# Optimization experiments

Hardware: AMD Instinct MI355X
Metric: run time of the kernel (lower is better)

Reference implementation:

```python
import jax, jax.numpy as jnp
import numpy as np

N = 5000
NUM_CLASSES = 81
BBOX_STD = jnp.array([0.1, 0.1, 0.2, 0.2], dtype=jnp.float32)
MIN_CONF = 0.7
MAX_INST = 100
NMS_THR = 0.3


def apply_box_delta(boxes, deltas):
    # boxes: [N,4] (y1,x1,y2,x2); deltas: [N,4] (dy,dx,log(dh),log(dw))
    h = boxes[:, 2] - boxes[:, 0]
    w = boxes[:, 3] - boxes[:, 1]
    cy = boxes[:, 0] + 0.5 * h
    cx = boxes[:, 1] + 0.5 * w
    cy = cy + deltas[:, 0] * h
    cx = cx + deltas[:, 1] * w
    h = h * jnp.exp(deltas[:, 2])
    w = w * jnp.exp(deltas[:, 3])
    y1 = cy - 0.5 * h
    x1 = cx - 0.5 * w
    return jnp.stack([y1, x1, y1 + h, x1 + w], axis=1)


def clip_boxes(boxes, window):
    wy1, wx1, wy2, wx2 = window[0], window[1], window[2], window[3]
    y1 = jnp.clip(boxes[:, 0], wy1, wy2)
    x1 = jnp.clip(boxes[:, 1], wx1, wx2)
    y2 = jnp.clip(boxes[:, 2], wy1, wy2)
    x2 = jnp.clip(boxes[:, 3], wx1, wx2)
    return jnp.stack([y1, x1, y2, x2], axis=1)


def pairwise_iou(boxes):
    # boxes: [N,4] -> iou: [N,N]
    y1, x1, y2, x2 = boxes[:, 0], boxes[:, 1], boxes[:, 2], boxes[:, 3]
    area = jnp.maximum(y2 - y1, 0.0) * jnp.maximum(x2 - x1, 0.0)
    iy1 = jnp.maximum(y1[:, None], y1[None, :])
    ix1 = jnp.maximum(x1[:, None], x1[None, :])
    iy2 = jnp.minimum(y2[:, None], y2[None, :])
    ix2 = jnp.minimum(x2[:, None], x2[None, :])
    inter = jnp.maximum(iy2 - iy1, 0.0) * jnp.maximum(ix2 - ix1, 0.0)
    union = area[:, None] + area[None, :] - inter
    return jnp.where(union > 0.0, inter / jnp.maximum(union, 1e-12), 0.0)


def setup_inputs() -> dict:
    key = jax.random.key(0)
    k1, k2, k3 = jax.random.split(key, 3)
    # valid boxes in normalized coords: (y1,x1) = min corner, (y2,x2) = max corner
    pts = jax.random.uniform(k1, (N, 2, 2), dtype=jnp.float32)
    lo = jnp.min(pts, axis=1)  # [N,2] -> (ymin, xmin)
    hi = jnp.max(pts, axis=1)  # [N,2] -> (ymax, xmax)
    ROIs = jnp.concatenate([lo, hi], axis=1)
    probs = jax.random.uniform(k2, (N, NUM_CLASSES), dtype=jnp.float32)
    deltas = jax.random.normal(k3, (N, NUM_CLASSES, 4), dtype=jnp.float32) * 0.5
    window = jnp.array([0.0, 0.0, 1.0, 1.0], dtype=jnp.float32)
    return {"ROIs": ROIs, "probs": probs, "deltas": deltas, "window": window}


def reference(ROIs, probs, deltas, window):
    n = probs.shape[0]
    rows = jnp.arange(n)
    # compute_delta: top class per ROI, its score and class-specific delta
    class_ids = jnp.argmax(probs, axis=1)
    class_scores = probs[rows, class_ids]
    deltas_specific = deltas[rows, class_ids] * BBOX_STD
    # refine + clip
    refined = clip_boxes(apply_box_delta(ROIs, deltas_specific), window)
    # keep: non-background & above confidence threshold
    valid = (class_ids > 0) & (class_scores >= MIN_CONF)
    # per-class greedy NMS, processed in global descending-score order
    # (identical result to per-unique-class tf.image.non_max_suppression)
    iou = pairwise_iou(refined)  # [N,N]
    neg_inf = jnp.float32(-jnp.inf)
    order = jnp.argsort(-jnp.where(valid, class_scores, neg_inf))

    def step(carry, i):
        kept, counts = carry
        c = class_ids[i]
        suppressed = jnp.any(kept & (class_ids == c) & (iou[i] > NMS_THR))
        ok = valid[i] & (~suppressed) & (counts[c] < MAX_INST)
        kept = kept.at[i].set(ok)
        counts = counts.at[c].add(ok.astype(jnp.int32))
        return (kept, counts), None

    init = (jnp.zeros((n,), dtype=bool), jnp.zeros((NUM_CLASSES,), dtype=jnp.int32))
    (kept, _), _ = jax.lax.scan(step, init, order)
    final = valid & kept
    # top detection_max_instances by score among surviving boxes
    masked_scores = jnp.where(final, class_scores, neg_inf)
    top_scores, top_ids = jax.lax.top_k(masked_scores, MAX_INST)
    ok = top_scores > neg_inf
    det = jnp.concatenate(
        [refined[top_ids],
         class_ids[top_ids].astype(jnp.float32)[:, None],
         class_scores[top_ids][:, None]], axis=1)
    # zero_pad_detections: invalid slots are zero
    return jnp.where(ok[:, None], det, 0.0)  # [MAX_INST, 6]
```

## Files before the change

### kernel.cpp

```cpp
#include <hip/hip_runtime.h>
#include <math.h>

#define NROI 5000
#define NCLS 81
#define MIN_CONF_F 0.7f
#define MAX_INST_I 100
#define NMS_THR_F 0.3f
#define CAP2 128
#define SURV_CAP 8192
#define HBINS 2048
#define CAPF 512
#define BMIN 0x3F333

__global__ __launch_bounds__(256) void det_stage1(
    const float* __restrict__ rois, const float* __restrict__ probs,
    const float* __restrict__ deltas, const float* __restrict__ window,
    float4* __restrict__ g_box, float* __restrict__ g_score,
    int* __restrict__ g_cid, unsigned int* __restrict__ ctrl)
{
  const int gtid = blockIdx.x * blockDim.x + threadIdx.x;
  if (gtid == 0) { ctrl[0] = 0u; ctrl[1] = 0u; }
  const int i = gtid >> 6;
  const int lane = threadIdx.x & 63;
  if (i >= NROI) return;
  const float* p = probs + (size_t)i * NCLS;
  float v0 = p[lane];
  unsigned long long key =
      ((unsigned long long)__float_as_uint(v0) << 32) | (unsigned)(255 - lane);
  if (lane < NCLS - 64) {
    float v1 = p[64 + lane];
    unsigned long long k1 =
        ((unsigned long long)__float_as_uint(v1) << 32) | (unsigned)(255 - (64 + lane));
    if (k1 > key) key = k1;
  }
  #pragma unroll
  for (int off = 32; off > 0; off >>= 1) {
    unsigned long long o = __shfl_xor(key, off, 64);
    if (o > key) key = o;
  }
  if (lane == 0) {
    int bc = 255 - (int)(key & 0xFFull);
    float best = __uint_as_float((unsigned)(key >> 32));
    const float* d = deltas + ((size_t)i * NCLS + bc) * 4;
    float dy = d[0]*0.1f, dx = d[1]*0.1f, dh = d[2]*0.2f, dwv = d[3]*0.2f;
    float y1 = rois[i*4+0], x1 = rois[i*4+1], y2 = rois[i*4+2], x2 = rois[i*4+3];
    float h = y2 - y1, w = x2 - x1;
    float cy = y1 + 0.5f*h, cx = x1 + 0.5f*w;
    cy = cy + dy*h; cx = cx + dx*w;
    h = h*expf(dh); w = w*expf(dwv);
    float ny1 = cy - 0.5f*h, nx1 = cx - 0.5f*w;
    float ny2 = ny1 + h, nx2 = nx1 + w;
    float wy1 = window[0], wx1 = window[1], wy2 = window[2], wx2 = window[3];
    ny1 = fminf(fmaxf(ny1, wy1), wy2);
    nx1 = fminf(fmaxf(nx1, wx1), wx2);
    ny2 = fminf(fmaxf(ny2, wy1), wy2);
    nx2 = fminf(fmaxf(nx2, wx1), wx2);
    g_box[i] = make_float4(ny1, nx1, ny2, nx2);
    g_score[i] = best;
    g_cid[i] = (bc > 0 && best >= MIN_CONF_F) ? bc : -1;
  }
}

__global__ __launch_bounds__(256) void det_nms_topk(
    const float4* __restrict__ g_box, const float* __restrict__ g_score,
    const int* __restrict__ g_cid, unsigned int* __restrict__ ctrl,
    unsigned long long* __restrict__ surv_key, int* __restrict__ surv_cid,
    float* __restrict__ out)
{
  const int c = blockIdx.x + 1;
  const int tid = threadIdx.x;
  __shared__ int scnt;
  __shared__ unsigned long long keys[CAP2], skey[CAP2];
  __shared__ float by1[CAP2], bx1[CAP2], by2[CAP2], bx2[CAP2], barea[CAP2];
  __shared__ unsigned int mask[CAP2][4];
  __shared__ unsigned char skept[CAP2];
  __shared__ int sticket;
  __shared__ int hist[HBINS];
  __shared__ unsigned long long cand[CAPF];
  __shared__ int csrc[CAPF];
  __shared__ float orows[6 * MAX_INST_I];
  __shared__ int wsum[4];
  __shared__ int fcnt, sR;

  if (tid == 0) scnt = 0;
  for (int q = tid; q < CAP2 * 4; q += 256) ((unsigned int*)mask)[q] = 0u;
  if (tid < CAP2) skept[tid] = 0;
  __syncthreads();
  const int4* cid4 = (const int4*)g_cid;
  for (int v = tid; v < NROI / 4; v += 256) {
    int4 cv = cid4[v];
    int base = v * 4;
    #pragma unroll
    for (int q = 0; q < 4; ++q) {
      int cq = (q == 0) ? cv.x : (q == 1) ? cv.y : (q == 2) ? cv.z : cv.w;
      if (cq == c) {
        int i = base + q;
        int pos = atomicAdd(&scnt, 1);
        if (pos < CAP2) {
          unsigned int sb = __float_as_uint(g_score[i]);
          keys[pos] = ((unsigned long long)sb << 32) |
                      (unsigned int)(0xFFFFFFFFu - (unsigned int)i);
        }
      }
    }
  }
  __syncthreads();
  int cnt = scnt < CAP2 ? scnt : CAP2;
  if (cnt > 0) {
    if (tid < cnt) {
      unsigned long long mk = keys[tid];
      int r = 0;
      for (int q = 0; q < cnt; ++q) r += (keys[q] > mk) ? 1 : 0;
      skey[r] = mk;
    }
    __syncthreads();
    if (tid < cnt) {
      int idx = (int)(0xFFFFFFFFu - (unsigned)(skey[tid] & 0xFFFFFFFFull));
      float4 b = g_box[idx];
      by1[tid] = b.x; bx1[tid] = b.y; by2[tid] = b.z; bx2[tid] = b.w;
      barea[tid] = fmaxf(b.z - b.x, 0.0f) * fmaxf(b.w - b.y, 0.0f);
    }
    __syncthreads();
    int m = 1, lg = 0;
    while (m < cnt) { m <<= 1; ++lg; }
    int tot = m * m;
    for (int p = tid; p < tot; p += 256) {
      int j = p >> lg, k = p & (m - 1);
      if (k > j && k < cnt) {
        float iy1 = fmaxf(by1[j], by1[k]);
        float ix1 = fmaxf(bx1[j], bx1[k]);
        float iy2 = fminf(by2[j], by2[k]);
        float ix2 = fminf(bx2[j], bx2[k]);
        float inter = fmaxf(iy2 - iy1, 0.0f) * fmaxf(ix2 - ix1, 0.0f);
        float uni = barea[j] + barea[k] - inter;
        float iou = (uni > 0.0f) ? inter / fmaxf(uni, 1e-12f) : 0.0f;
        if (iou > NMS_THR_F) atomicOr(&mask[j][k >> 5], 1u << (k & 31));
      }
    }
    __syncthreads();
    if (tid == 0) {
      unsigned long long rlo = 0ull, rhi = 0ull;
      int kc = 0;
      for (int j = 0; j < cnt; ++j) {
        unsigned int w0 = mask[j][0], w1 = mask[j][1], w2 = mask[j][2], w3 = mask[j][3];
        bool sup = (j < 64) ? (((rlo >> j) & 1ull) != 0)
                            : (((rhi >> (j - 64)) & 1ull) != 0);
        if (!sup && kc < MAX_INST_I) {
          skept[j] = 1; ++kc;
          rlo |= (unsigned long long)w0 | ((unsigned long long)w1 << 32);
          rhi |= (unsigned long long)w2 | ((unsigned long long)w3 << 32);
        }
      }
    }
    __syncthreads();
    if (tid < cnt && skept[tid]) {
      unsigned int pos = atomicAdd(&ctrl[0], 1u);
      if (pos < SURV_CAP) { surv_key[pos] = skey[tid]; surv_cid[pos] = c; }
    }
  }
  __syncthreads();
  if (tid == 0) {
    __threadfence();
    sticket = (int)atomicAdd(&ctrl[1], 1u);
  }
  __syncthreads();
  if (sticket != NCLS - 2) return;
  __threadfence();

  unsigned int n = atomicAdd(&ctrl[0], 0u);
  if (n > SURV_CAP) n = SURV_CAP;
  for (int b = tid; b < HBINS; b += 256) hist[b] = 0;
  if (tid == 0) { fcnt = 0; sR = 1 << 30; }
  for (int q = tid; q < 6 * MAX_INST_I; q += 256) orows[q] = 0.0f;
  __syncthreads();
  for (unsigned int i = tid; i < n; i += 256) {
    unsigned int bits = (unsigned int)(surv_key[i] >> 32);
    int b = (int)(bits >> 12) - BMIN;
    b = b < 0 ? 0 : (b > HBINS - 1 ? HBINS - 1 : b);
    atomicAdd(&hist[b], 1);
  }
  __syncthreads();
  int a[8]; int val = 0;
  #pragma unroll
  for (int q = 0; q < 8; ++q) { a[q] = hist[HBINS - 1 - (8 * tid + q)]; val += a[q]; }
  int incl = val;
  const int lane = tid & 63, wv = tid >> 6;
  #pragma unroll
  for (int off = 1; off < 64; off <<= 1) {
    int nn = __shfl_up(incl, off, 64);
    if (lane >= off) incl += nn;
  }
  if (lane == 63) wsum[wv] = incl;
  __syncthreads();
  if (tid == 0) { int s = 0; for (int q = 0; q < 4; ++q) { s += wsum[q]; wsum[q] = s; } }
  __syncthreads();
  incl += (wv > 0) ? wsum[wv - 1] : 0;
  int run = incl - val;
  #pragma unroll
  for (int q = 0; q < 8; ++q) {
    run += a[q];
    if (run >= MAX_INST_I) { atomicMin(&sR, 8 * tid + q); break; }
  }
  __syncthreads();
  const int T = (sR >= HBINS) ? 0 : (HBINS - 1 - sR);
  for (unsigned int i = tid; i < n; i += 256) {
    unsigned long long k = surv_key[i];
    unsigned int bits = (unsigned int)(k >> 32);
    int b = (int)(bits >> 12) - BMIN;
    b = b < 0 ? 0 : (b > HBINS - 1 ? HBINS - 1 : b);
    if (b >= T) {
      int pos = atomicAdd(&fcnt, 1);
      if (pos < CAPF) { cand[pos] = k; csrc[pos] = (int)i; }
    }
  }
  __syncthreads();
  int fc = fcnt < CAPF ? fcnt : CAPF;
  for (int e = tid; e < fc; e += 256) {
    unsigned long long mk = cand[e];
    int r = 0;
    for (int q = 0; q < fc; ++q) r += (cand[q] > mk) ? 1 : 0;
    if (r < MAX_INST_I) {
      int roi = (int)(0xFFFFFFFFu - (unsigned)(mk & 0xFFFFFFFFull));
      float4 b = g_box[roi];
      orows[r * 6 + 0] = b.x;
      orows[r * 6 + 1] = b.y;
      orows[r * 6 + 2] = b.z;
      orows[r * 6 + 3] = b.w;
      orows[r * 6 + 4] = (float)surv_cid[csrc[e]];
      orows[r * 6 + 5] = __uint_as_float((unsigned int)(mk >> 32));
    }
  }
  __syncthreads();
  for (int q = tid; q < 6 * MAX_INST_I; q += 256) out[q] = orows[q];
}

extern "C" void kernel_launch(void* const* d_in, const int* in_sizes, int n_in,
                              void* d_out, int out_size, void* d_ws, size_t ws_size,
                              hipStream_t stream)
{
  const float* rois   = (const float*)d_in[0];
  const float* probs  = (const float*)d_in[1];
  const float* deltas = (const float*)d_in[2];
  const float* window = (const float*)d_in[3];
  float* out = (float*)d_out;

  char* ws = (char*)d_ws;
  float4* g_box   = (float4*)ws;
  float*  g_score = (float*)(ws + 80000);
  int*    g_cid   = (int*)(ws + 100000);
  unsigned int* ctrl = (unsigned int*)(ws + 120000);
  unsigned long long* surv_key = (unsigned long long*)(ws + 120064);
  int* surv_cid = (int*)(ws + 120064 + SURV_CAP * 8);

  det_stage1<<<(NROI * 64 + 255) / 256, 256, 0, stream>>>(
      rois, probs, deltas, window, g_box, g_score, g_cid, ctrl);
  det_nms_topk<<<NCLS - 1, 256, 0, stream>>>(
      g_box, g_score, g_cid, ctrl, surv_key, surv_cid, out);
}
```

Measured before the change: 102.6 us.

## Fuse stages into one cooperative kernel with grid syncs

```diff
diff --git a/kernel.cpp b/kernel.cpp
--- a/kernel.cpp
+++ b/kernel.cpp
@@ -1,90 +1,88 @@
 #include <hip/hip_runtime.h>
+#include <hip/hip_cooperative_groups.h>
 #include <math.h>
+
+namespace cg = cooperative_groups;
 
 #define NROI 5000
 #define NCLS 81
 #define MIN_CONF_F 0.7f
 #define MAX_INST_I 100
 #define NMS_THR_F 0.3f
+#define NBLK 80
+#define NWAVE (NBLK * 4)
 #define CAP2 128
 #define SURV_CAP 8192
 #define HBINS 2048
 #define CAPF 512
 #define BMIN 0x3F333
 
-__global__ __launch_bounds__(256) void det_stage1(
+__global__ __launch_bounds__(256) void det_fused(
     const float* __restrict__ rois, const float* __restrict__ probs,
     const float* __restrict__ deltas, const float* __restrict__ window,
     float4* __restrict__ g_box, float* __restrict__ g_score,
-    int* __restrict__ g_cid, unsigned int* __restrict__ ctrl)
-{
-  const int gtid = blockIdx.x * blockDim.x + threadIdx.x;
-  if (gtid == 0) { ctrl[0] = 0u; ctrl[1] = 0u; }
-  const int i = gtid >> 6;
-  const int lane = threadIdx.x & 63;
-  if (i >= NROI) return;
-  const float* p = probs + (size_t)i * NCLS;
-  float v0 = p[lane];
-  unsigned long long key =
-      ((unsigned long long)__float_as_uint(v0) << 32) | (unsigned)(255 - lane);
-  if (lane < NCLS - 64) {
-    float v1 = p[64 + lane];
-    unsigned long long k1 =
-        ((unsigned long long)__float_as_uint(v1) << 32) | (unsigned)(255 - (64 + lane));
-    if (k1 > key) key = k1;
-  }
-  #pragma unroll
-  for (int off = 32; off > 0; off >>= 1) {
-    unsigned long long o = __shfl_xor(key, off, 64);
-    if (o > key) key = o;
-  }
-  if (lane == 0) {
-    int bc = 255 - (int)(key & 0xFFull);
-    float best = __uint_as_float((unsigned)(key >> 32));
-    const float* d = deltas + ((size_t)i * NCLS + bc) * 4;
-    float dy = d[0]*0.1f, dx = d[1]*0.1f, dh = d[2]*0.2f, dwv = d[3]*0.2f;
-    float y1 = rois[i*4+0], x1 = rois[i*4+1], y2 = rois[i*4+2], x2 = rois[i*4+3];
-    float h = y2 - y1, w = x2 - x1;
-    float cy = y1 + 0.5f*h, cx = x1 + 0.5f*w;
-    cy = cy + dy*h; cx = cx + dx*w;
-    h = h*expf(dh); w = w*expf(dwv);
-    float ny1 = cy - 0.5f*h, nx1 = cx - 0.5f*w;
-    float ny2 = ny1 + h, nx2 = nx1 + w;
-    float wy1 = window[0], wx1 = window[1], wy2 = window[2], wx2 = window[3];
-    ny1 = fminf(fmaxf(ny1, wy1), wy2);
-    nx1 = fminf(fmaxf(nx1, wx1), wx2);
-    ny2 = fminf(fmaxf(ny2, wy1), wy2);
-    nx2 = fminf(fmaxf(nx2, wx1), wx2);
-    g_box[i] = make_float4(ny1, nx1, ny2, nx2);
-    g_score[i] = best;
-    g_cid[i] = (bc > 0 && best >= MIN_CONF_F) ? bc : -1;
-  }
-}
-
-__global__ __launch_bounds__(256) void det_nms_topk(
-    const float4* __restrict__ g_box, const float* __restrict__ g_score,
-    const int* __restrict__ g_cid, unsigned int* __restrict__ ctrl,
+    int* __restrict__ g_cid, unsigned int* __restrict__ ctrl,
     unsigned long long* __restrict__ surv_key, int* __restrict__ surv_cid,
     float* __restrict__ out)
 {
+  cg::grid_group grid = cg::this_grid();
+  const int tid = threadIdx.x;
+  const int lane = tid & 63;
+  const int gw = blockIdx.x * 4 + (tid >> 6);
+
+  if (blockIdx.x == 0 && tid == 0) ctrl[0] = 0u;
+  for (int i = gw; i < NROI; i += NWAVE) {
+    const float* p = probs + (size_t)i * NCLS;
+    float v0 = p[lane];
+    unsigned long long key =
+        ((unsigned long long)__float_as_uint(v0) << 32) | (unsigned)(255 - lane);
+    if (lane < NCLS - 64) {
+      float v1 = p[64 + lane];
+      unsigned long long k1 =
+          ((unsigned long long)__float_as_uint(v1) << 32) | (unsigned)(255 - (64 + lane));
+      if (k1 > key) key = k1;
+    }
+    #pragma unroll
+    for (int off = 32; off > 0; off >>= 1) {
+      unsigned long long o = __shfl_xor(key, off, 64);
+      if (o > key) key = o;
+    }
+    if (lane == 0) {
+      int bc = 255 - (int)(key & 0xFFull);
+      float best = __uint_as_float((unsigned)(key >> 32));
+      const float* d = deltas + ((size_t)i * NCLS + bc) * 4;
+      float dy = d[0]*0.1f, dx = d[1]*0.1f, dh = d[2]*0.2f, dwv = d[3]*0.2f;
+      float y1 = rois[i*4+0], x1 = rois[i*4+1], y2 = rois[i*4+2], x2 = rois[i*4+3];
+      float h = y2 - y1, w = x2 - x1;
+      float cy = y1 + 0.5f*h, cx = x1 + 0.5f*w;
+      cy = cy + dy*h; cx = cx + dx*w;
+      h = h*expf(dh); w = w*expf(dwv);
+      float ny1 = cy - 0.5f*h, nx1 = cx - 0.5f*w;
+      float ny2 = ny1 + h, nx2 = nx1 + w;
+      float wy1 = window[0], wx1 = window[1], wy2 = window[2], wx2 = window[3];
+      ny1 = fminf(fmaxf(ny1, wy1), wy2);
+      nx1 = fminf(fmaxf(nx1, wx1), wx2);
+      ny2 = fminf(fmaxf(ny2, wy1), wy2);
+      nx2 = fminf(fmaxf(nx2, wx1), wx2);
+      g_box[i] = make_float4(ny1, nx1, ny2, nx2);
+      g_score[i] = best;
+      g_cid[i] = (bc > 0 && best >= MIN_CONF_F) ? bc : -1;
+    }
+  }
+  grid.sync();
+
   const int c = blockIdx.x + 1;
-  const int tid = threadIdx.x;
   __shared__ int scnt;
   __shared__ unsigned long long keys[CAP2], skey[CAP2];
   __shared__ float by1[CAP2], bx1[CAP2], by2[CAP2], bx2[CAP2], barea[CAP2];
   __shared__ unsigned int mask[CAP2][4];
-  __shared__ unsigned char skept[CAP2];
-  __shared__ int sticket;
-  __shared__ int hist[HBINS];
-  __shared__ unsigned long long cand[CAPF];
-  __shared__ int csrc[CAPF];
-  __shared__ float orows[6 * MAX_INST_I];
-  __shared__ int wsum[4];
-  __shared__ int fcnt, sR;
-
-  if (tid == 0) scnt = 0;
+  __shared__ int korder[CAP2];
+  __shared__ unsigned int sbase;
+  __shared__ int skc;
+
+  if (tid == 0) { scnt = 0; skc = 0; }
   for (int q = tid; q < CAP2 * 4; q += 256) ((unsigned int*)mask)[q] = 0u;
-  if (tid < CAP2) skept[tid] = 0;
+  if (tid < CAP2) korder[tid] = -1;
   __syncthreads();
   const int4* cid4 = (const int4*)g_cid;
   for (int v = tid; v < NROI / 4; v += 256) {
@@ -146,28 +144,31 @@
         bool sup = (j < 64) ? (((rlo >> j) & 1ull) != 0)
                             : (((rhi >> (j - 64)) & 1ull) != 0);
         if (!sup && kc < MAX_INST_I) {
-          skept[j] = 1; ++kc;
+          korder[j] = kc; ++kc;
           rlo |= (unsigned long long)w0 | ((unsigned long long)w1 << 32);
           rhi |= (unsigned long long)w2 | ((unsigned long long)w3 << 32);
         }
       }
-    }
-    __syncthreads();
-    if (tid < cnt && skept[tid]) {
-      unsigned int pos = atomicAdd(&ctrl[0], 1u);
-      if (pos < SURV_CAP) { surv_key[pos] = skey[tid]; surv_cid[pos] = c; }
-    }
-  }
-  __syncthreads();
-  if (tid == 0) {
-    __threadfence();
-    sticket = (int)atomicAdd(&ctrl[1], 1u);
-  }
-  __syncthreads();
-  if (sticket != NCLS - 2) return;
-  __threadfence();
-
-  unsigned int n = atomicAdd(&ctrl[0], 0u);
+      skc = kc;
+      sbase = kc ? atomicAdd(&ctrl[0], (unsigned)kc) : 0u;
+    }
+    __syncthreads();
+    if (tid < cnt && korder[tid] >= 0) {
+      unsigned int pos = sbase + (unsigned)korder[tid];
+      surv_key[pos] = skey[tid];
+      surv_cid[pos] = c;
+    }
+  }
+  grid.sync();
+
+  if (blockIdx.x != 0) return;
+  __shared__ int hist[HBINS];
+  __shared__ unsigned long long cand[CAPF];
+  __shared__ int csrc[CAPF];
+  __shared__ float orows[6 * MAX_INST_I];
+  __shared__ int wsum[4];
+  __shared__ int fcnt, sR;
+  unsigned int n = ctrl[0];
   if (n > SURV_CAP) n = SURV_CAP;
   for (int b = tid; b < HBINS; b += 256) hist[b] = 0;
   if (tid == 0) { fcnt = 0; sR = 1 << 30; }
@@ -184,7 +185,7 @@
   #pragma unroll
   for (int q = 0; q < 8; ++q) { a[q] = hist[HBINS - 1 - (8 * tid + q)]; val += a[q]; }
   int incl = val;
-  const int lane = tid & 63, wv = tid >> 6;
+  const int wv = tid >> 6;
   #pragma unroll
   for (int off = 1; off < 64; off <<= 1) {
     int nn = __shfl_up(incl, off, 64);
@@ -252,8 +253,9 @@
   unsigned long long* surv_key = (unsigned long long*)(ws + 120064);
   int* surv_cid = (int*)(ws + 120064 + SURV_CAP * 8);
 
-  det_stage1<<<(NROI * 64 + 255) / 256, 256, 0, stream>>>(
-      rois, probs, deltas, window, g_box, g_score, g_cid, ctrl);
-  det_nms_topk<<<NCLS - 1, 256, 0, stream>>>(
-      g_box, g_score, g_cid, ctrl, surv_key, surv_cid, out);
+  void* args[] = { (void*)&rois, (void*)&probs, (void*)&deltas, (void*)&window,
+                   (void*)&g_box, (void*)&g_score, (void*)&g_cid, (void*)&ctrl,
+                   (void*)&surv_key, (void*)&surv_cid, (void*)&out };
+  hipLaunchCooperativeKernel((const void*)det_fused, dim3(NBLK), dim3(256),
+                             args, 0, stream);
 }
```

After: 152.3 us. 1.49x slower.

## Split NMS and top-k into separate kernels with wave-parallel greedy scan

Applied to the files above, without the earlier changes.

```diff
diff --git a/kernel.cpp b/kernel.cpp
--- a/kernel.cpp
+++ b/kernel.cpp
@@ -7,7 +7,7 @@
 #define MAX_INST_I 100
 #define NMS_THR_F 0.3f
 #define CAP2 128
-#define SURV_CAP 8192
+#define SLOT 128
 #define HBINS 2048
 #define CAPF 512
 #define BMIN 0x3F333
@@ -16,10 +16,9 @@
     const float* __restrict__ rois, const float* __restrict__ probs,
     const float* __restrict__ deltas, const float* __restrict__ window,
     float4* __restrict__ g_box, float* __restrict__ g_score,
-    int* __restrict__ g_cid, unsigned int* __restrict__ ctrl)
+    int* __restrict__ g_cid)
 {
   const int gtid = blockIdx.x * blockDim.x + threadIdx.x;
-  if (gtid == 0) { ctrl[0] = 0u; ctrl[1] = 0u; }
   const int i = gtid >> 6;
   const int lane = threadIdx.x & 63;
   if (i >= NROI) return;
@@ -61,11 +60,11 @@
   }
 }
 
-__global__ __launch_bounds__(256) void det_nms_topk(
+__global__ __launch_bounds__(1024) void det_nms(
     const float4* __restrict__ g_box, const float* __restrict__ g_score,
-    const int* __restrict__ g_cid, unsigned int* __restrict__ ctrl,
-    unsigned long long* __restrict__ surv_key, int* __restrict__ surv_cid,
-    float* __restrict__ out)
+    const int* __restrict__ g_cid,
+    int* __restrict__ svc, unsigned long long* __restrict__ skeys,
+    float4* __restrict__ sboxes)
 {
   const int c = blockIdx.x + 1;
   const int tid = threadIdx.x;
@@ -73,34 +72,25 @@
   __shared__ unsigned long long keys[CAP2], skey[CAP2];
   __shared__ float by1[CAP2], bx1[CAP2], by2[CAP2], bx2[CAP2], barea[CAP2];
   __shared__ unsigned int mask[CAP2][4];
-  __shared__ unsigned char skept[CAP2];
-  __shared__ int sticket;
-  __shared__ int hist[HBINS];
-  __shared__ unsigned long long cand[CAPF];
-  __shared__ int csrc[CAPF];
-  __shared__ float orows[6 * MAX_INST_I];
-  __shared__ int wsum[4];
-  __shared__ int fcnt, sR;
-
+  __shared__ unsigned int keepw[4];
   if (tid == 0) scnt = 0;
-  for (int q = tid; q < CAP2 * 4; q += 256) ((unsigned int*)mask)[q] = 0u;
-  if (tid < CAP2) skept[tid] = 0;
+  for (int q = tid; q < CAP2 * 4; q += 1024) ((unsigned int*)mask)[q] = 0u;
   __syncthreads();
   const int4* cid4 = (const int4*)g_cid;
-  for (int v = tid; v < NROI / 4; v += 256) {
+  const float4* sc4 = (const float4*)g_score;
+  for (int v = tid; v < NROI / 4; v += 1024) {
     int4 cv = cid4[v];
+    float4 sv = sc4[v];
     int base = v * 4;
     #pragma unroll
     for (int q = 0; q < 4; ++q) {
       int cq = (q == 0) ? cv.x : (q == 1) ? cv.y : (q == 2) ? cv.z : cv.w;
+      float sq = (q == 0) ? sv.x : (q == 1) ? sv.y : (q == 2) ? sv.z : sv.w;
       if (cq == c) {
-        int i = base + q;
         int pos = atomicAdd(&scnt, 1);
-        if (pos < CAP2) {
-          unsigned int sb = __float_as_uint(g_score[i]);
-          keys[pos] = ((unsigned long long)sb << 32) |
-                      (unsigned int)(0xFFFFFFFFu - (unsigned int)i);
-        }
+        if (pos < CAP2)
+          keys[pos] = ((unsigned long long)__float_as_uint(sq) << 32) |
+                      (unsigned int)(0xFFFFFFFFu - (unsigned int)(base + q));
       }
     }
   }
@@ -124,7 +114,7 @@
     int m = 1, lg = 0;
     while (m < cnt) { m <<= 1; ++lg; }
     int tot = m * m;
-    for (int p = tid; p < tot; p += 256) {
+    for (int p = tid; p < tot; p += 1024) {
       int j = p >> lg, k = p & (m - 1);
       if (k > j && k < cnt) {
         float iy1 = fmaxf(by1[j], by1[k]);
@@ -137,54 +127,87 @@
         if (iou > NMS_THR_F) atomicOr(&mask[j][k >> 5], 1u << (k & 31));
       }
     }
-    __syncthreads();
+  }
+  __syncthreads();
+  if (tid < 64) {
+    unsigned long long row_lo = 0, row_hi = 0, row2_lo = 0, row2_hi = 0;
+    if (tid < cnt) {
+      row_lo = (unsigned long long)mask[tid][0] | ((unsigned long long)mask[tid][1] << 32);
+      row_hi = (unsigned long long)mask[tid][2] | ((unsigned long long)mask[tid][3] << 32);
+    }
+    if (tid + 64 < cnt) {
+      row2_lo = (unsigned long long)mask[tid+64][0] | ((unsigned long long)mask[tid+64][1] << 32);
+      row2_hi = (unsigned long long)mask[tid+64][2] | ((unsigned long long)mask[tid+64][3] << 32);
+    }
+    unsigned long long sup_lo = 0, sup_hi = 0, keep_lo = 0, keep_hi = 0;
+    int kc = 0;
+    for (int j = 0; j < cnt; ++j) {
+      bool s = (j < 64) ? (((sup_lo >> j) & 1ull) != 0)
+                        : (((sup_hi >> (j - 64)) & 1ull) != 0);
+      if (!s && kc < MAX_INST_I) {
+        if (j < 64) keep_lo |= 1ull << j; else keep_hi |= 1ull << (j - 64);
+        ++kc;
+        unsigned long long rl = (j < 64) ? row_lo : row2_lo;
+        unsigned long long rh = (j < 64) ? row_hi : row2_hi;
+        rl = __shfl(rl, j & 63, 64);
+        rh = __shfl(rh, j & 63, 64);
+        sup_lo |= rl; sup_hi |= rh;
+      }
+    }
     if (tid == 0) {
-      unsigned long long rlo = 0ull, rhi = 0ull;
-      int kc = 0;
-      for (int j = 0; j < cnt; ++j) {
-        unsigned int w0 = mask[j][0], w1 = mask[j][1], w2 = mask[j][2], w3 = mask[j][3];
-        bool sup = (j < 64) ? (((rlo >> j) & 1ull) != 0)
-                            : (((rhi >> (j - 64)) & 1ull) != 0);
-        if (!sup && kc < MAX_INST_I) {
-          skept[j] = 1; ++kc;
-          rlo |= (unsigned long long)w0 | ((unsigned long long)w1 << 32);
-          rhi |= (unsigned long long)w2 | ((unsigned long long)w3 << 32);
-        }
-      }
-    }
-    __syncthreads();
-    if (tid < cnt && skept[tid]) {
-      unsigned int pos = atomicAdd(&ctrl[0], 1u);
-      if (pos < SURV_CAP) { surv_key[pos] = skey[tid]; surv_cid[pos] = c; }
-    }
-  }
-  __syncthreads();
-  if (tid == 0) {
-    __threadfence();
-    sticket = (int)atomicAdd(&ctrl[1], 1u);
-  }
-  __syncthreads();
-  if (sticket != NCLS - 2) return;
-  __threadfence();
-
-  unsigned int n = atomicAdd(&ctrl[0], 0u);
-  if (n > SURV_CAP) n = SURV_CAP;
-  for (int b = tid; b < HBINS; b += 256) hist[b] = 0;
+      keepw[0] = (unsigned)keep_lo; keepw[1] = (unsigned)(keep_lo >> 32);
+      keepw[2] = (unsigned)keep_hi; keepw[3] = (unsigned)(keep_hi >> 32);
+      svc[c - 1] = kc;
+    }
+  }
+  __syncthreads();
+  if (tid < cnt) {
+    unsigned long long klo = (unsigned long long)keepw[0] | ((unsigned long long)keepw[1] << 32);
+    unsigned long long khi = (unsigned long long)keepw[2] | ((unsigned long long)keepw[3] << 32);
+    bool kept = (tid < 64) ? ((klo >> tid) & 1ull) : ((khi >> (tid - 64)) & 1ull);
+    if (kept) {
+      int order = (tid < 64)
+        ? __popcll(klo & ((1ull << tid) - 1ull))
+        : __popcll(klo) + __popcll(khi & ((1ull << (tid - 64)) - 1ull));
+      int slot = ((c - 1) << 7) + order;
+      skeys[slot] = skey[tid];
+      sboxes[slot] = make_float4(by1[tid], bx1[tid], by2[tid], bx2[tid]);
+    }
+  }
+}
+
+__global__ __launch_bounds__(1024) void det_topk(
+    const int* __restrict__ svc, const unsigned long long* __restrict__ skeys,
+    const float4* __restrict__ sboxes, float* __restrict__ out)
+{
+  const int tid = threadIdx.x;
+  const int lane = tid & 63, wv = tid >> 6;
+  __shared__ int svcnt[80];
+  __shared__ int hist[HBINS];
+  __shared__ unsigned long long cand[CAPF];
+  __shared__ int cslot[CAPF];
+  __shared__ float orows[6 * MAX_INST_I];
+  __shared__ int wsum[16];
+  __shared__ int fcnt, sR;
+  if (tid < 80) svcnt[tid] = svc[tid];
+  for (int b = tid; b < HBINS; b += 1024) hist[b] = 0;
   if (tid == 0) { fcnt = 0; sR = 1 << 30; }
-  for (int q = tid; q < 6 * MAX_INST_I; q += 256) orows[q] = 0.0f;
-  __syncthreads();
-  for (unsigned int i = tid; i < n; i += 256) {
-    unsigned int bits = (unsigned int)(surv_key[i] >> 32);
-    int b = (int)(bits >> 12) - BMIN;
-    b = b < 0 ? 0 : (b > HBINS - 1 ? HBINS - 1 : b);
-    atomicAdd(&hist[b], 1);
-  }
-  __syncthreads();
-  int a[8]; int val = 0;
-  #pragma unroll
-  for (int q = 0; q < 8; ++q) { a[q] = hist[HBINS - 1 - (8 * tid + q)]; val += a[q]; }
+  if (tid < 6 * MAX_INST_I) orows[tid] = 0.0f;
+  __syncthreads();
+  for (int s = tid; s < 80 * SLOT; s += 1024) {
+    int c = s >> 7, k = s & (SLOT - 1);
+    if (k < svcnt[c]) {
+      unsigned int bits = (unsigned int)(skeys[s] >> 32);
+      int b = (int)(bits >> 12) - BMIN;
+      b = b < 0 ? 0 : (b > HBINS - 1 ? HBINS - 1 : b);
+      atomicAdd(&hist[b], 1);
+    }
+  }
+  __syncthreads();
+  int a0 = hist[HBINS - 1 - 2 * tid];
+  int a1 = hist[HBINS - 2 - 2 * tid];
+  int val = a0 + a1;
   int incl = val;
-  const int lane = tid & 63, wv = tid >> 6;
   #pragma unroll
   for (int off = 1; off < 64; off <<= 1) {
     int nn = __shfl_up(incl, off, 64);
@@ -192,46 +215,46 @@
   }
   if (lane == 63) wsum[wv] = incl;
   __syncthreads();
-  if (tid == 0) { int s = 0; for (int q = 0; q < 4; ++q) { s += wsum[q]; wsum[q] = s; } }
+  if (tid == 0) { int s = 0; for (int q = 0; q < 16; ++q) { s += wsum[q]; wsum[q] = s; } }
   __syncthreads();
   incl += (wv > 0) ? wsum[wv - 1] : 0;
-  int run = incl - val;
-  #pragma unroll
-  for (int q = 0; q < 8; ++q) {
-    run += a[q];
-    if (run >= MAX_INST_I) { atomicMin(&sR, 8 * tid + q); break; }
-  }
+  int excl = incl - val;
+  if (excl + a0 >= MAX_INST_I) atomicMin(&sR, 2 * tid);
+  else if (incl >= MAX_INST_I) atomicMin(&sR, 2 * tid + 1);
   __syncthreads();
   const int T = (sR >= HBINS) ? 0 : (HBINS - 1 - sR);
-  for (unsigned int i = tid; i < n; i += 256) {
-    unsigned long long k = surv_key[i];
-    unsigned int bits = (unsigned int)(k >> 32);
-    int b = (int)(bits >> 12) - BMIN;
-    b = b < 0 ? 0 : (b > HBINS - 1 ? HBINS - 1 : b);
-    if (b >= T) {
-      int pos = atomicAdd(&fcnt, 1);
-      if (pos < CAPF) { cand[pos] = k; csrc[pos] = (int)i; }
+  for (int s = tid; s < 80 * SLOT; s += 1024) {
+    int c = s >> 7, k = s & (SLOT - 1);
+    if (k < svcnt[c]) {
+      unsigned long long key = skeys[s];
+      unsigned int bits = (unsigned int)(key >> 32);
+      int b = (int)(bits >> 12) - BMIN;
+      b = b < 0 ? 0 : (b > HBINS - 1 ? HBINS - 1 : b);
+      if (b >= T) {
+        int pos = atomicAdd(&fcnt, 1);
+        if (pos < CAPF) { cand[pos] = key; cslot[pos] = s; }
+      }
     }
   }
   __syncthreads();
   int fc = fcnt < CAPF ? fcnt : CAPF;
-  for (int e = tid; e < fc; e += 256) {
-    unsigned long long mk = cand[e];
+  if (tid < fc) {
+    unsigned long long mk = cand[tid];
     int r = 0;
     for (int q = 0; q < fc; ++q) r += (cand[q] > mk) ? 1 : 0;
     if (r < MAX_INST_I) {
-      int roi = (int)(0xFFFFFFFFu - (unsigned)(mk & 0xFFFFFFFFull));
-      float4 b = g_box[roi];
+      int slot = cslot[tid];
+      float4 b = sboxes[slot];
       orows[r * 6 + 0] = b.x;
       orows[r * 6 + 1] = b.y;
       orows[r * 6 + 2] = b.z;
       orows[r * 6 + 3] = b.w;
-      orows[r * 6 + 4] = (float)surv_cid[csrc[e]];
+      orows[r * 6 + 4] = (float)((slot >> 7) + 1);
       orows[r * 6 + 5] = __uint_as_float((unsigned int)(mk >> 32));
     }
   }
   __syncthreads();
-  for (int q = tid; q < 6 * MAX_INST_I; q += 256) out[q] = orows[q];
+  if (tid < 6 * MAX_INST_I) out[tid] = orows[tid];
 }
 
 extern "C" void kernel_launch(void* const* d_in, const int* in_sizes, int n_in,
@@ -248,12 +271,12 @@
   float4* g_box   = (float4*)ws;
   float*  g_score = (float*)(ws + 80000);
   int*    g_cid   = (int*)(ws + 100000);
-  unsigned int* ctrl = (unsigned int*)(ws + 120000);
-  unsigned long long* surv_key = (unsigned long long*)(ws + 120064);
-  int* surv_cid = (int*)(ws + 120064 + SURV_CAP * 8);
+  int*    svc     = (int*)(ws + 120000);
+  unsigned long long* skeys = (unsigned long long*)(ws + 120320);
+  float4* sboxes  = (float4*)(ws + 202240);
 
   det_stage1<<<(NROI * 64 + 255) / 256, 256, 0, stream>>>(
-      rois, probs, deltas, window, g_box, g_score, g_cid, ctrl);
-  det_nms_topk<<<NCLS - 1, 256, 0, stream>>>(
-      g_box, g_score, g_cid, ctrl, surv_key, surv_cid, out);
-}
+      rois, probs, deltas, window, g_box, g_score, g_cid);
+  det_nms<<<NCLS - 1, 1024, 0, stream>>>(g_box, g_score, g_cid, svc, skeys, sboxes);
+  det_topk<<<1, 1024, 0, stream>>>(svc, skeys, sboxes, out);
+}
```

After: 93.41 us, median of 2. 1.1x faster.
